# Optimization experiments

Measured on AMD Instinct MI355X. Metric: run time of the kernel, lower is better.

Reference implementation:

```python
import jax, jax.numpy as jnp
import numpy as np

TAU = 0.1
EPS = 1e-8  # torch CosineSimilarity eps


def setup_inputs() -> dict:
    key = jax.random.key(0)
    k1, k2, k3 = jax.random.split(key, 3)
    B, D = 4096, 128
    z_i = jax.random.normal(k1, (B, D), dtype=jnp.float32)
    z_j = jax.random.normal(k2, (B, D), dtype=jnp.float32)
    y = jax.random.randint(k3, (B,), 0, 2)
    return {"z_i": z_i, "z_j": z_j, "y": y}


def reference(z_i, z_j, y):
    # p: (N, D) with N = 2B
    p = jnp.concatenate([z_i, z_j], axis=0)
    # cosine similarity via row-normalization + matmul (same math as the
    # broadcasted torch CosineSimilarity, without the O(N^2*D) intermediate)
    norm = jnp.maximum(jnp.linalg.norm(p, axis=1, keepdims=True), EPS)
    pn = p / norm
    sim = jnp.einsum('id,jd->ij', pn, pn) / TAU  # (N, N)

    N = sim.shape[0]
    y2 = jnp.concatenate([y, y], axis=0)
    eye = jnp.eye(N, dtype=sim.dtype)
    pos_mask = (y2[:, None] == y2[None, :]).astype(sim.dtype) * (1.0 - eye)
    logit_mask = 1.0 - eye

    # denominator excludes the diagonal (self-similarity)
    exp_logits = jnp.exp(sim) * logit_mask
    log_prob = sim - jnp.log(jnp.sum(exp_logits, axis=1, keepdims=True))
    mean_log_prob_pos = jnp.sum(pos_mask * log_prob, axis=1) / jnp.sum(pos_mask, axis=1)
    loss = -jnp.sum(mean_log_prob_pos)
    return loss
```

## Files before the change

### kernel.cpp

```cpp
#include <hip/hip_runtime.h>
#include <math.h>

#define BSZ 4096
#define NROW 8192
#define DIM 128
#define LOG2E10 14.426950408889634f

typedef __attribute__((ext_vector_type(8))) short bf16x8;
typedef __attribute__((ext_vector_type(4))) float f32x4;

#define PNH_F     (NROW * DIM / 2)
#define G_OFF     (2 * PNH_F)
#define CNT_OFF   (G_OFF + 256)
#define SPART_OFF (G_OFF + 512)
#define PART_OFF  (SPART_OFF + 64 * NROW)

__device__ __forceinline__ unsigned short f2bf(float f) {
    unsigned u = __float_as_uint(f);
    return (unsigned short)((u + 0x7FFF + ((u >> 16) & 1)) >> 16);
}

__global__ void k_norm(const float* __restrict__ zi, const float* __restrict__ zj,
                       unsigned* __restrict__ pnh, unsigned* __restrict__ pnsw,
                       float* __restrict__ g) {
    int tid  = threadIdx.x;
    if (blockIdx.x == 0) g[tid] = 0.f;
    int wave = tid >> 6, lane = tid & 63;
    int row  = blockIdx.x * 4 + wave;
    const float* src = (row < BSZ) ? (zi + (size_t)row * DIM)
                                   : (zj + (size_t)(row - BSZ) * DIM);
    float2 v = ((const float2*)src)[lane];
    float ss = v.x * v.x + v.y * v.y;
    #pragma unroll
    for (int m = 32; m; m >>= 1) ss += __shfl_xor(ss, m, 64);
    float inv = 1.0f / fmaxf(sqrtf(ss), 1e-8f);
    unsigned short h0 = f2bf(v.x * inv), h1 = f2bf(v.y * inv);
    unsigned pack = (unsigned)h0 | ((unsigned)h1 << 16);
    pnh[(size_t)row * 64 + lane] = pack;
    int j = lane >> 2;
    int sw = ((j ^ (row & 15)) << 2) | (lane & 3);
    pnsw[(size_t)row * 64 + sw] = pack;
}

__global__ void k_colsum(const unsigned* __restrict__ pnh, const int* __restrict__ y,
                         float* __restrict__ g, float* __restrict__ cnt) {
    __shared__ float red[4][4][64];
    int tid = threadIdx.x;
    if (blockIdx.x < 128) {
        int d2 = tid & 63;
        int rg = tid >> 6;
        int row0 = blockIdx.x * 64 + rg * 16;
        float s0a = 0.f, s0b = 0.f, s1a = 0.f, s1b = 0.f;
        #pragma unroll 4
        for (int i = 0; i < 16; ++i) {
            int r = row0 + i;
            unsigned u = pnh[(size_t)r * 64 + d2];
            float va = __uint_as_float(u << 16);
            float vb = __uint_as_float(u & 0xFFFF0000u);
            if (y[r & (BSZ - 1)]) { s1a += va; s1b += vb; }
            else                  { s0a += va; s0b += vb; }
        }
        red[rg][0][d2] = s0a; red[rg][1][d2] = s0b;
        red[rg][2][d2] = s1a; red[rg][3][d2] = s1b;
        __syncthreads();
        int lab = tid >> 7, d = tid & 127;
        int which = lab * 2 + (d & 1), dd2 = d >> 1;
        float s = red[0][which][dd2] + red[1][which][dd2]
                + red[2][which][dd2] + red[3][which][dd2];
        atomicAdd(&g[lab * DIM + d], s);
    } else {
        __shared__ float r0[256];
        float c = 0.f;
        for (int r = tid; r < BSZ; r += 256) c += (float)y[r];
        r0[tid] = c;
        __syncthreads();
        for (int s = 128; s; s >>= 1) {
            if (tid < s) r0[tid] += r0[tid + s];
            __syncthreads();
        }
        if (tid == 0) { cnt[1] = 2.0f * r0[0]; cnt[0] = (float)NROW - 2.0f * r0[0]; }
    }
}

__global__ __launch_bounds__(256, 3)
void k_expsum(const unsigned short* __restrict__ pnsw, float* __restrict__ spart) {
    __shared__ short bt[128 * 128];
    int tid  = threadIdx.x;
    int lane = tid & 63;
    int w    = tid >> 6;
    int l15 = lane & 15, q = lane >> 4;
    int chunk = blockIdx.x;
    int rg    = blockIdx.y;
    int rwb   = rg * 256 + w * 64;

    {
        const float4* src = (const float4*)(pnsw + (size_t)chunk * 128 * DIM);
        float4* dst = (float4*)bt;
        #pragma unroll
        for (int i = 0; i < 8; ++i)
            dst[tid + 256 * i] = src[tid + 256 * i];
    }

    bf16x8 a[4][4];
    #pragma unroll
    for (int rf = 0; rf < 4; ++rf) {
        const unsigned short* ab = pnsw + (size_t)(rwb + rf * 16 + l15) * DIM;
        #pragma unroll
        for (int ks = 0; ks < 4; ++ks)
            a[rf][ks] = *(const bf16x8*)(ab + (((ks * 4 + q) ^ l15) << 3));
    }

    float rs[4][4];
    #pragma unroll
    for (int rf = 0; rf < 4; ++rf)
        #pragma unroll
        for (int e = 0; e < 4; ++e) rs[rf][e] = 0.f;

    __syncthreads();

    #pragma unroll
    for (int q4 = 0; q4 < 4; ++q4) {
        f32x4 acc[4][2];
        #pragma unroll
        for (int rf = 0; rf < 4; ++rf)
            #pragma unroll
            for (int cf = 0; cf < 2; ++cf) acc[rf][cf] = (f32x4){0.f, 0.f, 0.f, 0.f};

        #pragma unroll
        for (int ks = 0; ks < 4; ++ks)
            #pragma unroll
            for (int cf = 0; cf < 2; ++cf) {
                int brow = q4 * 32 + cf * 16 + l15;
                bf16x8 bfrag = *(const bf16x8*)(bt + brow * 128 + (((ks * 4 + q) ^ l15) << 3));
                #pragma unroll
                for (int rf = 0; rf < 4; ++rf)
                    acc[rf][cf] = __builtin_amdgcn_mfma_f32_16x16x32_bf16(a[rf][ks], bfrag, acc[rf][cf], 0, 0, 0);
            }

        #pragma unroll
        for (int cf = 0; cf < 2; ++cf) {
            int cb = chunk * 128 + q4 * 32 + cf * 16;
            bool dia = ((unsigned)(cb - rwb) < 64u);
            if (dia) {
                int col = cb + l15;
                #pragma unroll
                for (int rf = 0; rf < 4; ++rf)
                    #pragma unroll
                    for (int e = 0; e < 4; ++e) {
                        int row = rwb + rf * 16 + q * 4 + e;
                        float ex = exp2f(acc[rf][cf][e] * LOG2E10);
                        if (row == col) ex = 0.f;
                        rs[rf][e] += ex;
                    }
            } else {
                #pragma unroll
                for (int rf = 0; rf < 4; ++rf)
                    #pragma unroll
                    for (int e = 0; e < 4; ++e)
                        rs[rf][e] += exp2f(acc[rf][cf][e] * LOG2E10);
            }
        }
    }

    #pragma unroll
    for (int rf = 0; rf < 4; ++rf)
        #pragma unroll
        for (int e = 0; e < 4; ++e) {
            float v = rs[rf][e];
            v += __shfl_xor(v, 1, 16);
            v += __shfl_xor(v, 2, 16);
            v += __shfl_xor(v, 4, 16);
            v += __shfl_xor(v, 8, 16);
            if (l15 == 0)
                spart[(size_t)chunk * NROW + rwb + rf * 16 + q * 4 + e] = v;
        }
}

__global__ void k_finalize(const unsigned* __restrict__ pnh, const float* __restrict__ spart,
                           const float* __restrict__ g, const float* __restrict__ cnt,
                           const int* __restrict__ y, float* __restrict__ partial) {
    __shared__ float red[4];
    int tid = threadIdx.x, wv = tid >> 6, lane = tid & 63;
    int row = blockIdx.x * 4 + wv;
    int lab = y[row & (BSZ - 1)];
    unsigned u = pnh[(size_t)row * 64 + lane];
    float p0 = __uint_as_float(u << 16);
    float p1 = __uint_as_float(u & 0xFFFF0000u);
    float2 gv = ((const float2*)(g + lab * DIM))[lane];
    float dg = p0 * gv.x + p1 * gv.y;
    float ds = p0 * p0 + p1 * p1;
    float sp = spart[(size_t)lane * NROW + row];
    #pragma unroll
    for (int m = 32; m; m >>= 1) {
        dg += __shfl_xor(dg, m, 64);
        ds += __shfl_xor(ds, m, 64);
        sp += __shfl_xor(sp, m, 64);
    }
    if (lane == 0) {
        float C = cnt[lab] - 1.0f;
        float P = (dg - ds) * 10.0f;
        red[wv] = logf(sp) - P / C;
    }
    __syncthreads();
    if (tid == 0) partial[blockIdx.x] = red[0] + red[1] + red[2] + red[3];
}

__global__ void k_sum(const float* __restrict__ partial, float* __restrict__ out) {
    __shared__ float red[256];
    float v = 0.f;
    #pragma unroll
    for (int i = 0; i < 8; ++i) v += partial[threadIdx.x + 256 * i];
    red[threadIdx.x] = v;
    __syncthreads();
    for (int s = 128; s; s >>= 1) {
        if (threadIdx.x < s) red[threadIdx.x] += red[threadIdx.x + s];
        __syncthreads();
    }
    if (threadIdx.x == 0) out[0] = red[0];
}

extern "C" void kernel_launch(void* const* d_in, const int* in_sizes, int n_in,
                              void* d_out, int out_size, void* d_ws, size_t ws_size,
                              hipStream_t stream) {
    const float* zi = (const float*)d_in[0];
    const float* zj = (const float*)d_in[1];
    const int*   y  = (const int*)d_in[2];
    float* out = (float*)d_out;
    float* ws  = (float*)d_ws;

    unsigned* pnh   = (unsigned*)ws;
    unsigned* pnsw  = (unsigned*)(ws + PNH_F);
    float* g       = ws + G_OFF;
    float* cnt     = ws + CNT_OFF;
    float* spart   = ws + SPART_OFF;
    float* partial = ws + PART_OFF;

    k_norm<<<NROW / 4, 256, 0, stream>>>(zi, zj, pnh, pnsw, g);
    k_colsum<<<129, 256, 0, stream>>>(pnh, y, g, cnt);
    k_expsum<<<dim3(64, 32), 256, 0, stream>>>((const unsigned short*)pnsw, spart);
    k_finalize<<<NROW / 4, 256, 0, stream>>>(pnh, spart, g, cnt, y, partial);
    k_sum<<<1, 256, 0, stream>>>(partial, out);
}
```

Before: 114.3 us.

## Exploit similarity symmetry: compute upper-triangular tiles, emit row and column exp-sums

The exp-sum kernel now computes only the upper-triangular 128x128 tiles of the similarity matrix. Each tile's exponentials feed both its row sums and, through a shared-memory reduction, the transposed column sums, which roughly halves the MFMA and exp work. The log2(e)/tau scale is folded into a separately stored, pre-scaled bf16 copy of the A operand, removing a multiply per element. The costs are an extra normalized buffer write, column-sum reductions and LDS traffic, half the launched blocks exiting immediately, and a small asymmetry from rounding the scaled operand to bf16.

```diff
diff --git a/kernel.cpp b/kernel.cpp
--- a/kernel.cpp
+++ b/kernel.cpp
@@ -10,7 +10,9 @@
 typedef __attribute__((ext_vector_type(4))) float f32x4;
 
 #define PNH_F     (NROW * DIM / 2)
-#define G_OFF     (2 * PNH_F)
+#define PNSWB_OFF PNH_F
+#define PNSWA_OFF (2 * PNH_F)
+#define G_OFF     (3 * PNH_F)
 #define CNT_OFF   (G_OFF + 256)
 #define SPART_OFF (G_OFF + 512)
 #define PART_OFF  (SPART_OFF + 64 * NROW)
@@ -21,8 +23,8 @@
 }
 
 __global__ void k_norm(const float* __restrict__ zi, const float* __restrict__ zj,
-                       unsigned* __restrict__ pnh, unsigned* __restrict__ pnsw,
-                       float* __restrict__ g) {
+                       unsigned* __restrict__ pnh, unsigned* __restrict__ pnswB,
+                       unsigned* __restrict__ pnswA, float* __restrict__ g) {
     int tid  = threadIdx.x;
     if (blockIdx.x == 0) g[tid] = 0.f;
     int wave = tid >> 6, lane = tid & 63;
@@ -34,12 +36,14 @@
     #pragma unroll
     for (int m = 32; m; m >>= 1) ss += __shfl_xor(ss, m, 64);
     float inv = 1.0f / fmaxf(sqrtf(ss), 1e-8f);
-    unsigned short h0 = f2bf(v.x * inv), h1 = f2bf(v.y * inv);
-    unsigned pack = (unsigned)h0 | ((unsigned)h1 << 16);
+    float n0 = v.x * inv, n1 = v.y * inv;
+    unsigned pack  = (unsigned)f2bf(n0) | ((unsigned)f2bf(n1) << 16);
+    unsigned packA = (unsigned)f2bf(n0 * LOG2E10) | ((unsigned)f2bf(n1 * LOG2E10) << 16);
     pnh[(size_t)row * 64 + lane] = pack;
     int j = lane >> 2;
     int sw = ((j ^ (row & 15)) << 2) | (lane & 3);
-    pnsw[(size_t)row * 64 + sw] = pack;
+    pnswB[(size_t)row * 64 + sw] = pack;
+    pnswA[(size_t)row * 64 + sw] = packA;
 }
 
 __global__ void k_colsum(const unsigned* __restrict__ pnh, const int* __restrict__ y,
@@ -82,88 +86,89 @@
     }
 }
 
-__global__ __launch_bounds__(256, 3)
-void k_expsum(const unsigned short* __restrict__ pnsw, float* __restrict__ spart) {
+__global__ __launch_bounds__(256, 4)
+void k_expsum(const unsigned short* __restrict__ pnswA,
+              const unsigned short* __restrict__ pnswB,
+              float* __restrict__ spart) {
+    int ti = blockIdx.y, tj = blockIdx.x;
+    if (tj < ti) return;
     __shared__ short bt[128 * 128];
+    __shared__ float rs_t[128];
+    __shared__ float cs_p[4][128];
     int tid  = threadIdx.x;
     int lane = tid & 63;
     int w    = tid >> 6;
     int l15 = lane & 15, q = lane >> 4;
-    int chunk = blockIdx.x;
-    int rg    = blockIdx.y;
-    int rwb   = rg * 256 + w * 64;
+    bool isDiag = (ti == tj);
+    int rwb = ti * 128 + w * 32;
 
     {
-        const float4* src = (const float4*)(pnsw + (size_t)chunk * 128 * DIM);
+        const float4* src = (const float4*)(pnswB + (size_t)tj * 128 * DIM);
         float4* dst = (float4*)bt;
         #pragma unroll
         for (int i = 0; i < 8; ++i)
             dst[tid + 256 * i] = src[tid + 256 * i];
     }
 
-    bf16x8 a[4][4];
-    #pragma unroll
-    for (int rf = 0; rf < 4; ++rf) {
-        const unsigned short* ab = pnsw + (size_t)(rwb + rf * 16 + l15) * DIM;
+    bf16x8 a[2][4];
+    #pragma unroll
+    for (int rf = 0; rf < 2; ++rf) {
+        const unsigned short* ab = pnswA + (size_t)(rwb + rf * 16 + l15) * DIM;
         #pragma unroll
         for (int ks = 0; ks < 4; ++ks)
             a[rf][ks] = *(const bf16x8*)(ab + (((ks * 4 + q) ^ l15) << 3));
     }
 
-    float rs[4][4];
-    #pragma unroll
-    for (int rf = 0; rf < 4; ++rf)
+    float rs[2][4], cs[8];
+    #pragma unroll
+    for (int rf = 0; rf < 2; ++rf)
         #pragma unroll
         for (int e = 0; e < 4; ++e) rs[rf][e] = 0.f;
-
-    __syncthreads();
-
-    #pragma unroll
-    for (int q4 = 0; q4 < 4; ++q4) {
-        f32x4 acc[4][2];
-        #pragma unroll
-        for (int rf = 0; rf < 4; ++rf)
+    #pragma unroll
+    for (int t = 0; t < 8; ++t) cs[t] = 0.f;
+
+    __syncthreads();
+
+    #pragma unroll
+    for (int t = 0; t < 8; ++t) {
+        bf16x8 b[4];
+        #pragma unroll
+        for (int ks = 0; ks < 4; ++ks)
+            b[ks] = *(const bf16x8*)(bt + (t * 16 + l15) * 128 + (((ks * 4 + q) ^ l15) << 3));
+
+        f32x4 acc[2];
+        acc[0] = (f32x4){0.f, 0.f, 0.f, 0.f};
+        acc[1] = (f32x4){0.f, 0.f, 0.f, 0.f};
+        #pragma unroll
+        for (int ks = 0; ks < 4; ++ks) {
+            acc[0] = __builtin_amdgcn_mfma_f32_16x16x32_bf16(a[0][ks], b[ks], acc[0], 0, 0, 0);
+            acc[1] = __builtin_amdgcn_mfma_f32_16x16x32_bf16(a[1][ks], b[ks], acc[1], 0, 0, 0);
+        }
+
+        if (isDiag && ((unsigned)(t * 16 - w * 32) < 32u)) {
+            int col = tj * 128 + t * 16 + l15;
             #pragma unroll
-            for (int cf = 0; cf < 2; ++cf) acc[rf][cf] = (f32x4){0.f, 0.f, 0.f, 0.f};
-
-        #pragma unroll
-        for (int ks = 0; ks < 4; ++ks)
+            for (int rf = 0; rf < 2; ++rf)
+                #pragma unroll
+                for (int e = 0; e < 4; ++e) {
+                    int row = rwb + rf * 16 + q * 4 + e;
+                    float ex = exp2f(acc[rf][e]);
+                    if (row == col) ex = 0.f;
+                    rs[rf][e] += ex; cs[t] += ex;
+                }
+        } else {
             #pragma unroll
-            for (int cf = 0; cf < 2; ++cf) {
-                int brow = q4 * 32 + cf * 16 + l15;
-                bf16x8 bfrag = *(const bf16x8*)(bt + brow * 128 + (((ks * 4 + q) ^ l15) << 3));
+            for (int rf = 0; rf < 2; ++rf)
                 #pragma unroll
-                for (int rf = 0; rf < 4; ++rf)
-                    acc[rf][cf] = __builtin_amdgcn_mfma_f32_16x16x32_bf16(a[rf][ks], bfrag, acc[rf][cf], 0, 0, 0);
-            }
-
-        #pragma unroll
-        for (int cf = 0; cf < 2; ++cf) {
-            int cb = chunk * 128 + q4 * 32 + cf * 16;
-            bool dia = ((unsigned)(cb - rwb) < 64u);
-            if (dia) {
-                int col = cb + l15;
-                #pragma unroll
-                for (int rf = 0; rf < 4; ++rf)
-                    #pragma unroll
-                    for (int e = 0; e < 4; ++e) {
-                        int row = rwb + rf * 16 + q * 4 + e;
-                        float ex = exp2f(acc[rf][cf][e] * LOG2E10);
-                        if (row == col) ex = 0.f;
-                        rs[rf][e] += ex;
-                    }
-            } else {
-                #pragma unroll
-                for (int rf = 0; rf < 4; ++rf)
-                    #pragma unroll
-                    for (int e = 0; e < 4; ++e)
-                        rs[rf][e] += exp2f(acc[rf][cf][e] * LOG2E10);
-            }
-        }
-    }
-
-    #pragma unroll
-    for (int rf = 0; rf < 4; ++rf)
+                for (int e = 0; e < 4; ++e) {
+                    float ex = exp2f(acc[rf][e]);
+                    rs[rf][e] += ex; cs[t] += ex;
+                }
+        }
+    }
+
+    #pragma unroll
+    for (int rf = 0; rf < 2; ++rf)
         #pragma unroll
         for (int e = 0; e < 4; ++e) {
             float v = rs[rf][e];
@@ -171,9 +176,24 @@
             v += __shfl_xor(v, 2, 16);
             v += __shfl_xor(v, 4, 16);
             v += __shfl_xor(v, 8, 16);
-            if (l15 == 0)
-                spart[(size_t)chunk * NROW + rwb + rf * 16 + q * 4 + e] = v;
-        }
+            if (l15 == 0) rs_t[w * 32 + rf * 16 + q * 4 + e] = v;
+        }
+    #pragma unroll
+    for (int t = 0; t < 8; ++t) {
+        float v = cs[t];
+        v += __shfl_xor(v, 16, 64);
+        v += __shfl_xor(v, 32, 64);
+        if (q == 0) cs_p[w][t * 16 + l15] = v;
+    }
+    __syncthreads();
+
+    if (tid < 128) {
+        spart[(size_t)tj * NROW + ti * 128 + tid] = rs_t[tid];
+    } else if (!isDiag) {
+        int c = tid - 128;
+        float v = cs_p[0][c] + cs_p[1][c] + cs_p[2][c] + cs_p[3][c];
+        spart[(size_t)ti * NROW + tj * 128 + c] = v;
+    }
 }
 
 __global__ void k_finalize(const unsigned* __restrict__ pnh, const float* __restrict__ spart,
@@ -229,15 +249,17 @@
     float* ws  = (float*)d_ws;
 
     unsigned* pnh   = (unsigned*)ws;
-    unsigned* pnsw  = (unsigned*)(ws + PNH_F);
+    unsigned* pnswB = (unsigned*)(ws + PNSWB_OFF);
+    unsigned* pnswA = (unsigned*)(ws + PNSWA_OFF);
     float* g       = ws + G_OFF;
     float* cnt     = ws + CNT_OFF;
     float* spart   = ws + SPART_OFF;
     float* partial = ws + PART_OFF;
 
-    k_norm<<<NROW / 4, 256, 0, stream>>>(zi, zj, pnh, pnsw, g);
+    k_norm<<<NROW / 4, 256, 0, stream>>>(zi, zj, pnh, pnswB, pnswA, g);
     k_colsum<<<129, 256, 0, stream>>>(pnh, y, g, cnt);
-    k_expsum<<<dim3(64, 32), 256, 0, stream>>>((const unsigned short*)pnsw, spart);
+    k_expsum<<<dim3(64, 64), 256, 0, stream>>>((const unsigned short*)pnswA,
+                                               (const unsigned short*)pnswB, spart);
     k_finalize<<<NROW / 4, 256, 0, stream>>>(pnh, spart, g, cnt, y, partial);
     k_sum<<<1, 256, 0, stream>>>(partial, out);
 }
```

Measured after the change: 100.7 us. 1.13x faster.
